# Optimization experiments

Hardware: AMD Instinct MI355X
Metric: run time of the kernel (lower is better)

The kernel has to match this reference:

```python
import jax, jax.numpy as jnp
import numpy as np

C = 384  # model channels

def generate_path(duration, mask):
    # duration: [B, Tp] int; mask: [B, Tp, Tf] float -> 0/1 path [B, Tp, Tf]
    cum = jnp.cumsum(duration, axis=-1)                     # [B, Tp]
    frames = jnp.arange(mask.shape[-1])                     # [Tf]
    path = (frames[None, None, :] < cum[:, :, None]).astype(mask.dtype)
    path = path - jnp.pad(path, ((0, 0), (1, 0), (0, 0)))[:, :-1]
    return path * mask


def setup_inputs() -> dict:
    key = jax.random.key(0)
    ks = jax.random.split(key, 16)
    B, Tp, Tf = 32, 512, 2048
    s = 1.0 / np.sqrt(C)
    inp = {
        "x": jax.random.normal(ks[0], (B, C, Tp), jnp.float32),
        "phone_mask": jnp.ones((B, 1, Tp), jnp.float32),
        "frame_mask": jnp.ones((B, 1, Tf), jnp.float32),
        "duration": jax.random.randint(ks[1], (B, 1, Tp), 0, 4, jnp.int32),
        "log_cf0": jax.random.normal(ks[2], (B, 1, Tf), jnp.float32),
        "vuv": jax.random.uniform(ks[3], (B, 1, Tf), jnp.float32),
        "energy": jax.random.normal(ks[4], (B, 1, Tf), jnp.float32),
        # learned params (1x1 conv == per-timestep linear)
        "dur_w": jax.random.normal(ks[5], (1, C), jnp.float32) * s,
        "dur_b": jnp.zeros((1,), jnp.float32),
        "pitch_w": jax.random.normal(ks[6], (2, C), jnp.float32) * s,
        "pitch_b": jnp.zeros((2,), jnp.float32),
        "pemb_w": jax.random.normal(ks[7], (C, 1), jnp.float32),
        "pemb_b": jnp.zeros((C,), jnp.float32),
        "enp_w": jax.random.normal(ks[8], (1, C), jnp.float32) * s,
        "enp_b": jnp.zeros((1,), jnp.float32),
        "eemb_w": jax.random.normal(ks[9], (C, 1), jnp.float32),
        "eemb_b": jnp.zeros((C,), jnp.float32),
    }
    return inp


def reference(x, phone_mask, frame_mask, duration, log_cf0, vuv, energy,
              dur_w, dur_b, pitch_w, pitch_b, pemb_w, pemb_b,
              enp_w, enp_b, eemb_w, eemb_b):
    # duration predictor (masked 1x1 conv): [B,1,Tp]
    log_duration_pred = (jnp.einsum('bct,oc->bot', x, dur_w) + dur_b[None, :, None]) * phone_mask

    # path_mask [B,Tp,Tf] = phone_mask (x) frame_mask
    path_mask = phone_mask[:, 0, :, None] * frame_mask[:, 0, None, :]
    attn_path = generate_path(duration[:, 0, :], path_mask)        # [B,Tp,Tf]

    # length regulation: [B,C,Tp] @ [B,Tp,Tf] -> [B,C,Tf]
    xf = jnp.einsum('bcp,bpf->bcf', x, attn_path.astype(x.dtype))

    # pitch predictor -> split channels into log_cf0_pred / vuv_pred
    pv = (jnp.einsum('bct,oc->bot', xf, pitch_w) + pitch_b[None, :, None]) * frame_mask
    log_cf0_pred, vuv_pred = pv[:, 0:1], pv[:, 1:2]

    # masked pitch embedding add: 1 -> C projection of ground-truth log_cf0
    pitch_emb = (jnp.einsum('bit,ci->bct', log_cf0, pemb_w) + pemb_b[None, :, None]) * frame_mask

    # energy predictor + masked energy embedding
    energy_pred = (jnp.einsum('bct,oc->bot', xf, enp_w) + enp_b[None, :, None]) * frame_mask
    energy_emb = (jnp.einsum('bit,ci->bct', energy, eemb_w) + eemb_b[None, :, None]) * frame_mask

    out = xf + pitch_emb + energy_emb
    return (out, log_duration_pred, log_cf0_pred, vuv_pred, energy_pred)
```

## Files before the change

kernel.cpp:

```cpp
#include <hip/hip_runtime.h>

#define BB 32
#define CC 384
#define TP 512
#define TF 2048

typedef float f32x4 __attribute__((ext_vector_type(4)));

__device__ __forceinline__ void nt_store4f(float* p, float4 v) {
    f32x4 t = {v.x, v.y, v.z, v.w};
    __builtin_nontemporal_store(t, (f32x4*)p);
}
__device__ __forceinline__ int imax(int a, int b) { return a > b ? a : b; }
__device__ __forceinline__ int imin(int a, int b) { return a < b ? a : b; }

__global__ __launch_bounds__(256) void mono_kernel(
    const float* __restrict__ x, const float* __restrict__ phone_mask,
    const float* __restrict__ frame_mask, const int* __restrict__ duration,
    const float* __restrict__ log_cf0, const float* __restrict__ energy,
    const float* __restrict__ dur_w, const float* __restrict__ dur_b,
    const float* __restrict__ pitch_w, const float* __restrict__ pitch_b,
    const float* __restrict__ pemb_w, const float* __restrict__ pemb_b,
    const float* __restrict__ enp_w, const float* __restrict__ enp_b,
    const float* __restrict__ eemb_w, const float* __restrict__ eemb_b,
    float* __restrict__ out, float* __restrict__ ldp, float* __restrict__ lcp,
    float* __restrict__ vup, float* __restrict__ epp) {
    int b = blockIdx.y;
    int j = blockIdx.x;
    int tid = threadIdx.x;
    int lane = tid & 63;
    int wv = tid >> 6;
    const float* xb = x + (size_t)b * CC * TP;

    if (j < 24) {
        __shared__ int po[TF];
        __shared__ int ps[256];
        __shared__ float pm_s[TP];
        __shared__ float xs[16 * TP];
        int c0 = __builtin_amdgcn_readfirstlane(j * 16);
        const float* src = xb + (size_t)c0 * TP;
#pragma unroll
        for (int q = 0; q < 8; ++q)
            *(float4*)(xs + tid * 32 + 4 * q) = *(const float4*)(src + tid * 32 + 4 * q);

        int d0 = duration[b * TP + 2 * tid];
        int d1 = duration[b * TP + 2 * tid + 1];
        ps[tid] = d0 + d1;
        pm_s[tid] = phone_mask[b * TP + tid];
        pm_s[tid + 256] = phone_mask[b * TP + tid + 256];
#pragma unroll
        for (int h = 0; h < 8; ++h) po[tid + 256 * h] = -1;
        __syncthreads();
        for (int off = 1; off < 256; off <<= 1) {
            int v = (tid >= off) ? ps[tid - off] : 0;
            __syncthreads();
            ps[tid] += v;
            __syncthreads();
        }
        int excl = tid ? ps[tid - 1] : 0;
        int e0 = imin(excl + d0, TF);
        int e1 = imin(excl + d0 + d1, TF);
        for (int f = imin(excl, TF); f < e0; ++f) po[f] = 2 * tid;
        for (int f = e0; f < e1; ++f) po[f] = 2 * tid + 1;
        __syncthreads();

        float wA[16], wB[16], wC[16];
#pragma unroll
        for (int r = 0; r < 16; ++r) {
            wA[r] = pemb_w[c0 + r];
            wB[r] = pemb_b[c0 + r] + eemb_b[c0 + r];
            wC[r] = eemb_w[c0 + r];
        }
        const float* fm_b = frame_mask + (size_t)b * TF;
        const float* lc_b = log_cf0 + (size_t)b * TF;
        const float* en_b = energy + (size_t)b * TF;
        float* ob = out + ((size_t)b * CC + c0) * TF;
        int fbase = wv * 512;

#pragma unroll
        for (int it = 0; it < 2; ++it) {
            int f0 = fbase + it * 256 + 4 * lane;
            int4 p4 = *(const int4*)(po + f0);
            float4 fm4 = *(const float4*)(fm_b + f0);
            float4 lc4 = *(const float4*)(lc_b + f0);
            float4 en4 = *(const float4*)(en_b + f0);
            int4 pc;
            pc.x = imax(p4.x, 0); pc.y = imax(p4.y, 0);
            pc.z = imax(p4.z, 0); pc.w = imax(p4.w, 0);
            float4 xm4;
            xm4.x = (p4.x >= 0 ? pm_s[pc.x] : 0.f) * fm4.x;
            xm4.y = (p4.y >= 0 ? pm_s[pc.y] : 0.f) * fm4.y;
            xm4.z = (p4.z >= 0 ? pm_s[pc.z] : 0.f) * fm4.z;
            xm4.w = (p4.w >= 0 ? pm_s[pc.w] : 0.f) * fm4.w;
            float lcx = lc4.x * fm4.x, lcy = lc4.y * fm4.y, lcz = lc4.z * fm4.z, lcw = lc4.w * fm4.w;
            float enx = en4.x * fm4.x, eny = en4.y * fm4.y, enz = en4.z * fm4.z, enw = en4.w * fm4.w;
#pragma unroll
            for (int r = 0; r < 16; ++r) {
                const float* xsr = xs + r * TP;
                float4 o;
                o.x = xsr[pc.x] * xm4.x + lcx * wA[r] + enx * wC[r] + fm4.x * wB[r];
                o.y = xsr[pc.y] * xm4.y + lcy * wA[r] + eny * wC[r] + fm4.y * wB[r];
                o.z = xsr[pc.z] * xm4.z + lcz * wA[r] + enz * wC[r] + fm4.z * wB[r];
                o.w = xsr[pc.w] * xm4.w + lcw * wA[r] + enw * wC[r] + fm4.w * wB[r];
                nt_store4f(ob + (size_t)r * TF + f0, o);
            }
        }
    } else {
        int jj = j - 24;
        __shared__ float r[16 * 64];
        __shared__ int ps[256];
        __shared__ float y_lds[3 * 64];
        __shared__ float pm_lds[64];
        __shared__ short po_win[192];
        int t = jj * 64 + lane;
        float a0 = 0.f, a1 = 0.f, a2 = 0.f, a3 = 0.f;
#pragma unroll 8
        for (int i = 0; i < CC / 4; ++i) {
            int c = __builtin_amdgcn_readfirstlane(wv + 4 * i);
            float xv = xb[c * TP + t];
            a0 += xv * pitch_w[c];
            a1 += xv * pitch_w[CC + c];
            a2 += xv * enp_w[c];
            a3 += xv * dur_w[c];
        }
        r[(0 * 4 + wv) * 64 + lane] = a0;
        r[(1 * 4 + wv) * 64 + lane] = a1;
        r[(2 * 4 + wv) * 64 + lane] = a2;
        r[(3 * 4 + wv) * 64 + lane] = a3;
        int d0 = duration[b * TP + 2 * tid];
        int d1 = duration[b * TP + 2 * tid + 1];
        ps[tid] = d0 + d1;
        if (tid < 64) pm_lds[tid] = phone_mask[b * TP + jj * 64 + tid];
        __syncthreads();
        for (int off = 1; off < 256; off <<= 1) {
            int v = (tid >= off) ? ps[tid - off] : 0;
            __syncthreads();
            ps[tid] += v;
            __syncthreads();
        }
        float a = 0.f;
#pragma unroll
        for (int k = 0; k < 4; ++k) a += r[(wv * 4 + k) * 64 + lane];
        if (wv == 3)
            ldp[b * TP + t] = (a + dur_b[0]) * pm_lds[lane];
        else
            y_lds[wv * 64 + lane] = a;
        int base_lo = (jj > 0) ? imin(ps[jj * 32 - 1], TF) : 0;
        int base_hi = imin(ps[(jj + 1) * 32 - 1], TF);
        if (tid >= jj * 32 && tid < (jj + 1) * 32) {
            int excl = tid ? ps[tid - 1] : 0;
            int e0 = imin(excl + d0, TF);
            int e1 = imin(excl + d0 + d1, TF);
            for (int f = imin(excl, TF); f < e0; ++f) po_win[f - base_lo] = (short)(2 * tid - jj * 64);
            for (int f = e0; f < e1; ++f) po_win[f - base_lo] = (short)(2 * tid + 1 - jj * 64);
        }
        int total = imin(ps[255], TF);
        __syncthreads();
        int win = base_hi - base_lo;
        for (int idx = tid; idx < win; idx += 256) {
            int f = base_lo + idx;
            int p = po_win[idx];
            float fm = frame_mask[b * TF + f];
            float xm = pm_lds[p] * fm;
            lcp[b * TF + f] = (y_lds[p] * xm + pitch_b[0]) * fm;
            vup[b * TF + f] = (y_lds[64 + p] * xm + pitch_b[1]) * fm;
            epp[b * TF + f] = (y_lds[128 + p] * xm + enp_b[0]) * fm;
        }
        if (jj == 7) {
            for (int f = total + tid; f < TF; f += 256) {
                float fm = frame_mask[b * TF + f];
                lcp[b * TF + f] = pitch_b[0] * fm;
                vup[b * TF + f] = pitch_b[1] * fm;
                epp[b * TF + f] = enp_b[0] * fm;
            }
        }
    }
}

extern "C" void kernel_launch(void* const* d_in, const int* in_sizes, int n_in,
                              void* d_out, int out_size, void* d_ws, size_t ws_size,
                              hipStream_t stream) {
    const float* x          = (const float*)d_in[0];
    const float* phone_mask = (const float*)d_in[1];
    const float* frame_mask = (const float*)d_in[2];
    const int*   duration   = (const int*)d_in[3];
    const float* log_cf0    = (const float*)d_in[4];
    const float* energy     = (const float*)d_in[6];
    const float* dur_w      = (const float*)d_in[7];
    const float* dur_b      = (const float*)d_in[8];
    const float* pitch_w    = (const float*)d_in[9];
    const float* pitch_b    = (const float*)d_in[10];
    const float* pemb_w     = (const float*)d_in[11];
    const float* pemb_b     = (const float*)d_in[12];
    const float* enp_w      = (const float*)d_in[13];
    const float* enp_b      = (const float*)d_in[14];
    const float* eemb_w     = (const float*)d_in[15];
    const float* eemb_b     = (const float*)d_in[16];

    float* out = (float*)d_out;
    float* ldp = out + (size_t)BB * CC * TF;
    float* lcp = ldp + (size_t)BB * TP;
    float* vup = lcp + (size_t)BB * TF;
    float* epp = vup + (size_t)BB * TF;

    mono_kernel<<<dim3(32, BB), dim3(256), 0, stream>>>(
        x, phone_mask, frame_mask, duration, log_cf0, energy, dur_w, dur_b,
        pitch_w, pitch_b, pemb_w, pemb_b, enp_w, enp_b, eemb_w, eemb_b,
        out, ldp, lcp, vup, epp);
}
```

Measured before the change: 31.43 us.

## Pre-mask x in LDS, use short index map, scalar coalesced gather stores

The channel-tile branch now multiplies x by phone_mask while loading it into LDS. This drops the separate pm_s array and the per-frame mask lookup. The frame-to-phone index map shrinks to 16-bit shorts, duration is loaded as int2, and launch bounds now request 4 blocks per CU. The output loop switches from float4 stores of 4 consecutive frames to scalar nontemporal stores at a 64-frame stride, so each lane's LDS gathers hit different banks. In exchange, each thread issues four times as many store instructions.

```diff
diff --git a/kernel.cpp b/kernel.cpp
--- a/kernel.cpp
+++ b/kernel.cpp
@@ -7,14 +7,10 @@
 
 typedef float f32x4 __attribute__((ext_vector_type(4)));
 
-__device__ __forceinline__ void nt_store4f(float* p, float4 v) {
-    f32x4 t = {v.x, v.y, v.z, v.w};
-    __builtin_nontemporal_store(t, (f32x4*)p);
-}
 __device__ __forceinline__ int imax(int a, int b) { return a > b ? a : b; }
 __device__ __forceinline__ int imin(int a, int b) { return a < b ? a : b; }
 
-__global__ __launch_bounds__(256) void mono_kernel(
+__global__ __launch_bounds__(256, 4) void mono_kernel(
     const float* __restrict__ x, const float* __restrict__ phone_mask,
     const float* __restrict__ frame_mask, const int* __restrict__ duration,
     const float* __restrict__ log_cf0, const float* __restrict__ energy,
@@ -33,23 +29,26 @@
     const float* xb = x + (size_t)b * CC * TP;
 
     if (j < 24) {
-        __shared__ int po[TF];
+        __shared__ short po16[TF];
         __shared__ int ps[256];
-        __shared__ float pm_s[TP];
         __shared__ float xs[16 * TP];
         int c0 = __builtin_amdgcn_readfirstlane(j * 16);
         const float* src = xb + (size_t)c0 * TP;
-#pragma unroll
-        for (int q = 0; q < 8; ++q)
-            *(float4*)(xs + tid * 32 + 4 * q) = *(const float4*)(src + tid * 32 + 4 * q);
-
-        int d0 = duration[b * TP + 2 * tid];
-        int d1 = duration[b * TP + 2 * tid + 1];
+        const float* pmb = phone_mask + (size_t)b * TP;
+#pragma unroll
+        for (int q = 0; q < 8; ++q) {
+            int off = q * 1024 + tid * 4;
+            float4 v = *(const float4*)(src + off);
+            float4 m = *(const float4*)(pmb + (off & (TP - 1)));
+            v.x *= m.x; v.y *= m.y; v.z *= m.z; v.w *= m.w;
+            *(float4*)(xs + off) = v;
+        }
+
+        int2 d01 = *(const int2*)(duration + b * TP + 2 * tid);
+        int d0 = d01.x, d1 = d01.y;
         ps[tid] = d0 + d1;
-        pm_s[tid] = phone_mask[b * TP + tid];
-        pm_s[tid + 256] = phone_mask[b * TP + tid + 256];
-#pragma unroll
-        for (int h = 0; h < 8; ++h) po[tid + 256 * h] = -1;
+#pragma unroll
+        for (int h = 0; h < 4; ++h) ((int*)po16)[tid + 256 * h] = -1;
         __syncthreads();
         for (int off = 1; off < 256; off <<= 1) {
             int v = (tid >= off) ? ps[tid - off] : 0;
@@ -60,8 +59,8 @@
         int excl = tid ? ps[tid - 1] : 0;
         int e0 = imin(excl + d0, TF);
         int e1 = imin(excl + d0 + d1, TF);
-        for (int f = imin(excl, TF); f < e0; ++f) po[f] = 2 * tid;
-        for (int f = e0; f < e1; ++f) po[f] = 2 * tid + 1;
+        for (int f = imin(excl, TF); f < e0; ++f) po16[f] = (short)(2 * tid);
+        for (int f = e0; f < e1; ++f) po16[f] = (short)(2 * tid + 1);
         __syncthreads();
 
         float wA[16], wB[16], wC[16];
@@ -79,30 +78,31 @@
 
 #pragma unroll
         for (int it = 0; it < 2; ++it) {
-            int f0 = fbase + it * 256 + 4 * lane;
-            int4 p4 = *(const int4*)(po + f0);
-            float4 fm4 = *(const float4*)(fm_b + f0);
-            float4 lc4 = *(const float4*)(lc_b + f0);
-            float4 en4 = *(const float4*)(en_b + f0);
-            int4 pc;
-            pc.x = imax(p4.x, 0); pc.y = imax(p4.y, 0);
-            pc.z = imax(p4.z, 0); pc.w = imax(p4.w, 0);
-            float4 xm4;
-            xm4.x = (p4.x >= 0 ? pm_s[pc.x] : 0.f) * fm4.x;
-            xm4.y = (p4.y >= 0 ? pm_s[pc.y] : 0.f) * fm4.y;
-            xm4.z = (p4.z >= 0 ? pm_s[pc.z] : 0.f) * fm4.z;
-            xm4.w = (p4.w >= 0 ? pm_s[pc.w] : 0.f) * fm4.w;
-            float lcx = lc4.x * fm4.x, lcy = lc4.y * fm4.y, lcz = lc4.z * fm4.z, lcw = lc4.w * fm4.w;
-            float enx = en4.x * fm4.x, eny = en4.y * fm4.y, enz = en4.z * fm4.z, enw = en4.w * fm4.w;
+            int f0 = fbase + it * 256 + lane;
+            int p[4], pcl[4];
+            float fmv[4], lcv[4], env[4];
+#pragma unroll
+            for (int k = 0; k < 4; ++k) {
+                int f = f0 + 64 * k;
+                p[k] = po16[f];
+                pcl[k] = imax(p[k], 0);
+                fmv[k] = fm_b[f];
+                lcv[k] = lc_b[f];
+                env[k] = en_b[f];
+            }
 #pragma unroll
             for (int r = 0; r < 16; ++r) {
                 const float* xsr = xs + r * TP;
-                float4 o;
-                o.x = xsr[pc.x] * xm4.x + lcx * wA[r] + enx * wC[r] + fm4.x * wB[r];
-                o.y = xsr[pc.y] * xm4.y + lcy * wA[r] + eny * wC[r] + fm4.y * wB[r];
-                o.z = xsr[pc.z] * xm4.z + lcz * wA[r] + enz * wC[r] + fm4.z * wB[r];
-                o.w = xsr[pc.w] * xm4.w + lcw * wA[r] + enw * wC[r] + fm4.w * wB[r];
-                nt_store4f(ob + (size_t)r * TF + f0, o);
+                float* obr = ob + (size_t)r * TF + f0;
+#pragma unroll
+                for (int k = 0; k < 4; ++k) {
+                    float xv = xsr[pcl[k]];
+                    float v = (p[k] >= 0) ? xv : 0.f;
+                    float t = __builtin_fmaf(lcv[k], wA[r], wB[r]);
+                    t = __builtin_fmaf(env[k], wC[r], t);
+                    float o = (v + t) * fmv[k];
+                    __builtin_nontemporal_store(o, obr + 64 * k);
+                }
             }
         }
     } else {
@@ -127,8 +127,8 @@
         r[(1 * 4 + wv) * 64 + lane] = a1;
         r[(2 * 4 + wv) * 64 + lane] = a2;
         r[(3 * 4 + wv) * 64 + lane] = a3;
-        int d0 = duration[b * TP + 2 * tid];
-        int d1 = duration[b * TP + 2 * tid + 1];
+        int2 d01 = *(const int2*)(duration + b * TP + 2 * tid);
+        int d0 = d01.x, d1 = d01.y;
         ps[tid] = d0 + d1;
         if (tid < 64) pm_lds[tid] = phone_mask[b * TP + jj * 64 + tid];
         __syncthreads();
```

Result: no change. 31.66 us (+0.7%).
